# Kernel optimization log

Hardware: AMD Instinct MI355X
Metric: run time of the kernel (lower is better)

The kernel has to match this reference:

```python
import jax, jax.numpy as jnp
import numpy as np

EPS = 1e-07


def _softsplat(tenIn, tenFlow):
    # tenIn: [N, C, H, W], tenFlow: [N, 2, H, W]
    N, C, H, W = tenIn.shape
    dtype = tenIn.dtype
    gridX = jnp.arange(W, dtype=dtype)[None, None, :]  # [1,1,W]
    gridY = jnp.arange(H, dtype=dtype)[None, :, None]  # [1,H,1]
    fltX = gridX + tenFlow[:, 0]  # [N,H,W]
    fltY = gridY + tenFlow[:, 1]  # [N,H,W]
    finite = jnp.isfinite(fltX) & jnp.isfinite(fltY)
    fltX = jnp.where(finite, fltX, 0.0)
    fltY = jnp.where(finite, fltY, 0.0)
    nwX = jnp.floor(fltX)
    nwY = jnp.floor(fltY)
    b = jnp.arange(N, dtype=jnp.int32)[:, None, None]  # [N,1,1]
    tenIn_flat = jnp.transpose(tenIn, (0, 2, 3, 1)).reshape(-1, C)  # [N*H*W, C]
    out = jnp.zeros((N * H * W, C), dtype=dtype)
    # four bilinear corners: NW, NE, SW, SE
    for dx, dy in ((0, 0), (1, 0), (0, 1), (1, 1)):
        ix = nwX + dx
        iy = nwY + dy
        # bilinear weight, e.g. NW: (nwX+1-fltX)*(nwY+1-fltY)
        w = (1.0 - jnp.abs(fltX - ix)) * (1.0 - jnp.abs(fltY - iy))
        valid = finite & (ix >= 0) & (ix < W) & (iy >= 0) & (iy < H)
        w = jnp.where(valid, w, 0.0)  # zero-weight replaces torch's masked select
        ixi = jnp.clip(ix.astype(jnp.int32), 0, W - 1)
        iyi = jnp.clip(iy.astype(jnp.int32), 0, H - 1)
        idx = (b * (H * W) + iyi * W + ixi).reshape(-1)  # [N*H*W]
        out = out.at[idx].add(tenIn_flat * w.reshape(-1, 1))
    return jnp.transpose(out.reshape(N, H, W, C), (0, 3, 1, 2))


def setup_inputs() -> dict:
    key = jax.random.key(0)
    k1, k2, k3 = jax.random.split(key, 3)
    N, C, H, W = 4, 3, 1080, 1920
    tenIn = jax.random.normal(k1, (N, C, H, W), dtype=jnp.float32)
    tenFlow = jax.random.normal(k2, (N, 2, H, W), dtype=jnp.float32)
    tenMetric = jax.random.normal(k3, (N, 1, H, W), dtype=jnp.float32)
    return {"tenIn": tenIn, "tenFlow": tenFlow, "tenMetric": tenMetric}


def reference(tenIn, tenFlow, tenMetric):
    # mode='soft': concat [tenIn * exp(metric), exp(metric)], splat, normalize
    m = jnp.exp(tenMetric)
    tenCat = jnp.concatenate([tenIn * m, m], axis=1)  # [N, C+1, H, W]
    tenOut = _softsplat(tenCat, tenFlow)
    # mode_sub is None -> addeps normalization
    return tenOut[:, :-1] / (tenOut[:, -1:] + EPS)
```

## Files before the change

### kernel.cpp

```cpp
#include <hip/hip_runtime.h>
#include <math.h>

#define EPS 1e-7f

constexpr int Nn = 4, Hh = 1080, Ww = 1920;
constexpr int HW = Hh * Ww;
constexpr int TOTAL = Nn * HW;

constexpr int TW = 32, TH = 32;
constexpr int TXN = 60, TYN = 34;
constexpr int REACH = 5;
constexpr float NEAR_MAX = 5.0f;
constexpr int WINW = TW + 2 * REACH;
constexpr int WINH = TH + 2 * REACH;
constexpr int WINSZ = WINW * WINH;
constexpr int NCH = TH + 1;
constexpr int NCWc = TW + 1;
constexpr int NCELLS = NCWc * NCH;
constexpr int NOFF = NCELLS + 1;
constexpr int PADL = 8;
constexpr int NCHUNK = 12;
constexpr int TOTCH = NCHUNK * WINH;
constexpr float INV64K = 1.52587890625e-5f;


__global__ __launch_bounds__(256) void far_scatter(
    const float* __restrict__ tenIn, const float* __restrict__ tenFlow,
    const float* __restrict__ tenMetric,
    unsigned int* __restrict__ farCount, float* __restrict__ farList,
    unsigned int farCap)
{
    int q = blockIdx.x * 256 + threadIdx.x;
    if (q >= TOTAL / 4) return;
    int n  = q / (HW / 4);
    int p  = (q - n * (HW / 4)) * 4;

    const float* __restrict__ f0 = tenFlow + (size_t)(n * 2 + 0) * HW;
    const float* __restrict__ f1 = f0 + HW;
    float4 fx4 = *(const float4*)(f0 + p);
    float4 fy4 = *(const float4*)(f1 + p);

    float mx = fmaxf(fmaxf(fabsf(fx4.x), fabsf(fx4.y)), fmaxf(fabsf(fx4.z), fabsf(fx4.w)));
    float my = fmaxf(fmaxf(fabsf(fy4.x), fabsf(fy4.y)), fmaxf(fabsf(fy4.z), fabsf(fy4.w)));
    if (!(mx > NEAR_MAX || my > NEAR_MAX)) return;

    int y = p / Ww;
    int xbase = p - y * Ww;
    float fxa[4] = {fx4.x, fx4.y, fx4.z, fx4.w};
    float fya[4] = {fy4.x, fy4.y, fy4.z, fy4.w};

#pragma unroll
    for (int k = 0; k < 4; ++k) {
        float fxv = fxa[k], fyv = fya[k];
        if (!(fabsf(fxv) > NEAR_MAX || fabsf(fyv) > NEAR_MAX)) continue;
        float fx = (float)(xbase + k) + fxv;
        float fy = (float)y + fyv;
        if (!isfinite(fx) || !isfinite(fy)) continue;
        if (!(fx > -1.0f && fx < (float)Ww && fy > -1.0f && fy < (float)Hh)) continue;

        int pp = p + k;
        float m  = expf(tenMetric[(size_t)n * HW + pp]);
        float v0 = tenIn[((size_t)n * 3 + 0) * HW + pp] * m;
        float v1 = tenIn[((size_t)n * 3 + 1) * HW + pp] * m;
        float v2 = tenIn[((size_t)n * 3 + 2) * HW + pp] * m;

        unsigned int slot = atomicAdd(farCount, 1u);
        if (slot < farCap) {
            float* ep = farList + (size_t)slot * 8;
            ep[0] = __int_as_float(n);
            ep[1] = fx; ep[2] = fy;
            ep[3] = v0; ep[4] = v1; ep[5] = v2; ep[6] = m;
            ep[7] = 0.0f;
        }
    }
}


__global__ __launch_bounds__(256, 4) void gather_splat(
    const float* __restrict__ tenIn, const float* __restrict__ tenFlow,
    const float* __restrict__ tenMetric,
    const float* __restrict__ farList, const unsigned int* __restrict__ farCount,
    unsigned int farCap, float* __restrict__ out)
{
    __shared__ float4 sVal[WINSZ];
    __shared__ unsigned int sPack[WINSZ];
    __shared__ unsigned int sOff[NOFF];
    __shared__ unsigned int sWsum[8];

    const int tx = blockIdx.x, ty = blockIdx.y, n = blockIdx.z;
    const int tX = tx * TW, tY = ty * TH;
    const int tid = threadIdx.x;

    for (int j = tid; j < NOFF; j += 256) sOff[j] = 0u;
    __syncthreads();

    const float* __restrict__ f0 = tenFlow   + (size_t)(n * 2 + 0) * HW;
    const float* __restrict__ f1 = tenFlow   + (size_t)(n * 2 + 1) * HW;
    const float* __restrict__ mp = tenMetric + (size_t)n * HW;
    const float* __restrict__ i0 = tenIn + (size_t)(n * 3 + 0) * HW;
    const float* __restrict__ i1 = tenIn + (size_t)(n * 3 + 1) * HW;
    const float* __restrict__ i2 = tenIn + (size_t)(n * 3 + 2) * HW;

    unsigned int pk[2][4];
    unsigned int spw[2][4];
    float rv0[2][4], rv1[2][4], rv2[2][4], rvm[2][4];

#pragma unroll
    for (int cc = 0; cc < 2; ++cc) {
#pragma unroll
        for (int k = 0; k < 4; ++k) pk[cc][k] = 0xFFFFFFFFu;
        int cidx = tid + cc * 256;
        if (cidx >= TOTCH) continue;
        int wy = cidx / NCHUNK;
        int cx = cidx - wy * NCHUNK;
        int sy = tY - REACH + wy;
        int gx = tX - PADL + cx * 4;
        if (sy < 0 || sy >= Hh || gx < 0 || gx > Ww - 4) continue;
        int p = sy * Ww + gx;
        float4 fx4 = *(const float4*)(f0 + p);
        float4 fy4 = *(const float4*)(f1 + p);
        float4 m4  = *(const float4*)(mp + p);
        float4 a04 = *(const float4*)(i0 + p);
        float4 a14 = *(const float4*)(i1 + p);
        float4 a24 = *(const float4*)(i2 + p);
        float fxa[4] = {fx4.x, fx4.y, fx4.z, fx4.w};
        float fya[4] = {fy4.x, fy4.y, fy4.z, fy4.w};
        float ma[4]  = {m4.x,  m4.y,  m4.z,  m4.w};
        float a0a[4] = {a04.x, a04.y, a04.z, a04.w};
        float a1a[4] = {a14.x, a14.y, a14.z, a14.w};
        float a2a[4] = {a24.x, a24.y, a24.z, a24.w};
#pragma unroll
        for (int k = 0; k < 4; ++k) {
            int x = gx + k;
            if (x < tX - REACH || x >= tX + TW + REACH) continue;
            float fxv = fxa[k], fyv = fya[k];
            if (!(fabsf(fxv) <= NEAR_MAX && fabsf(fyv) <= NEAR_MAX)) continue;
            float fx = (float)x + fxv;
            float fy = (float)sy + fyv;
            float flx = floorf(fx), fly = floorf(fy);
            int lx0 = (int)flx - tX;
            int ly0 = (int)fly - tY;
            if (lx0 < -1 || lx0 >= TW || ly0 < -1 || ly0 >= TH) continue;
            int ci = (lx0 + 1) * NCH + (ly0 + 1);
            unsigned int sic = atomicAdd(&sOff[ci], 1u);
            pk[cc][k] = (sic << 16) | (unsigned int)ci;
            spw[cc][k] = __float2uint_rz((fx - flx) * 65536.0f)
                       | (__float2uint_rz((fy - fly) * 65536.0f) << 16);
            float m = expf(ma[k]);
            rv0[cc][k] = a0a[k] * m;
            rv1[cc][k] = a1a[k] * m;
            rv2[cc][k] = a2a[k] * m;
            rvm[cc][k] = m;
        }
    }
    __syncthreads();

    unsigned int c0v = 0, c1v = 0, c2v = 0, c3v = 0, c4v = 0;
    if (tid < 218) {
        int base = tid * 5;
        c0v = sOff[base];     c1v = sOff[base + 1]; c2v = sOff[base + 2];
        c3v = sOff[base + 3]; c4v = sOff[base + 4];
    }
    unsigned int tsum = c0v + c1v + c2v + c3v + c4v;
    unsigned int incl = tsum;
#pragma unroll
    for (int d = 1; d < 64; d <<= 1) {
        unsigned int v = __shfl_up(incl, d);
        if ((tid & 63) >= d) incl += v;
    }
    const int wv = tid >> 6;
    if ((tid & 63) == 63) sWsum[wv] = incl;
    __syncthreads();
    unsigned int woff = 0;
    {
        unsigned int w0 = sWsum[0], w1 = sWsum[1], w2 = sWsum[2];
        if (wv > 0) woff += w0;
        if (wv > 1) woff += w1;
        if (wv > 2) woff += w2;
    }
    unsigned int texcl = woff + incl - tsum;
    if (tid < 218) {
        int base = tid * 5;
        unsigned int o0 = texcl, o1 = o0 + c0v, o2 = o1 + c1v, o3 = o2 + c2v, o4 = o3 + c3v;
        sOff[base] = o0; sOff[base + 1] = o1; sOff[base + 2] = o2;
        sOff[base + 3] = o3; sOff[base + 4] = o4;
    }
    __syncthreads();

#pragma unroll
    for (int cc = 0; cc < 2; ++cc) {
#pragma unroll
        for (int k = 0; k < 4; ++k) {
            unsigned int p_ = pk[cc][k];
            if (p_ == 0xFFFFFFFFu) continue;
            unsigned int ci  = p_ & 0xFFFFu;
            unsigned int sic = p_ >> 16;
            unsigned int slot = sOff[ci] + sic;
            sPack[slot] = spw[cc][k];
            sVal[slot]  = make_float4(rv0[cc][k], rv1[cc][k], rv2[cc][k], rvm[cc][k]);
        }
    }
    __syncthreads();

    const int r   = tid >> 3;
    const int g   = tid & 7;
    const int cc0 = g * 4;

    float4 acc0 = make_float4(0.f, 0.f, 0.f, 0.f);
    float4 acc1 = make_float4(0.f, 0.f, 0.f, 0.f);
    float4 acc2 = make_float4(0.f, 0.f, 0.f, 0.f);
    float4 acc3 = make_float4(0.f, 0.f, 0.f, 0.f);

#define COLRANGE(J, HASL, HASR, ACCL, ACCR)                               \
    {                                                                     \
        const int cbase = (cc0 + (J)) * NCH + r;                          \
        unsigned int lo = sOff[cbase], md = sOff[cbase + 1],              \
                     hi = sOff[cbase + 2];                                \
        for (unsigned int s = lo; s < hi; ++s) {                          \
            unsigned int pw = sPack[s];                                   \
            float4 v = sVal[s];                                           \
            float fracx = (float)(pw & 0xFFFFu) * INV64K;                 \
            float wy1q  = (float)(pw >> 16)     * INV64K;                 \
            float ay = (s < md) ? wy1q : (1.0f - wy1q);                   \
            float wr = ay * fracx;                                        \
            float wl = ay - wr;                                           \
            if (HASL) { ACCL.x += v.x*wl; ACCL.y += v.y*wl;               \
                        ACCL.z += v.z*wl; ACCL.w += v.w*wl; }             \
            if (HASR) { ACCR.x += v.x*wr; ACCR.y += v.y*wr;               \
                        ACCR.z += v.z*wr; ACCR.w += v.w*wr; }             \
        }                                                                 \
    }

    COLRANGE(0, false, true,  acc0, acc0)
    COLRANGE(1, true,  true,  acc0, acc1)
    COLRANGE(2, true,  true,  acc1, acc2)
    COLRANGE(3, true,  true,  acc2, acc3)
    COLRANGE(4, true,  false, acc3, acc0)
#undef COLRANGE

    const int gy = tY + r;
    if (gy >= Hh) return;
    const int gx = tX + cc0;

    unsigned int fc = *farCount;
    if (fc > farCap) fc = farCap;
    const float gyf = (float)gy;
    const float gxf = (float)gx;
    for (unsigned int e = 0; e < fc; ++e) {
        const float* ep = farList + (size_t)e * 8;
        if (__float_as_int(ep[0]) != n) continue;
        float ffx = ep[1], ffy = ep[2];
        float ay = fmaxf(0.f, 1.f - fabsf(ffy - gyf));
        if (ay > 0.f) {
            float fv0 = ep[3], fv1 = ep[4], fv2 = ep[5], fm = ep[6];
            float d = ffx - gxf;
            float ax0 = fmaxf(0.f, 1.f - fabsf(d));
            float ax1 = fmaxf(0.f, 1.f - fabsf(d - 1.f));
            float ax2 = fmaxf(0.f, 1.f - fabsf(d - 2.f));
            float ax3 = fmaxf(0.f, 1.f - fabsf(d - 3.f));
            float w0 = ay * ax0, w1 = ay * ax1, w2 = ay * ax2, w3 = ay * ax3;
            acc0.x += fv0 * w0; acc0.y += fv1 * w0; acc0.z += fv2 * w0; acc0.w += fm * w0;
            acc1.x += fv0 * w1; acc1.y += fv1 * w1; acc1.z += fv2 * w1; acc1.w += fm * w1;
            acc2.x += fv0 * w2; acc2.y += fv1 * w2; acc2.z += fv2 * w2; acc2.w += fm * w2;
            acc3.x += fv0 * w3; acc3.y += fv1 * w3; acc3.z += fv2 * w3; acc3.w += fm * w3;
        }
    }

    const float inv0 = 1.0f / (acc0.w + EPS);
    const float inv1 = 1.0f / (acc1.w + EPS);
    const float inv2 = 1.0f / (acc2.w + EPS);
    const float inv3 = 1.0f / (acc3.w + EPS);

    const size_t pix = (size_t)gy * Ww + gx;
    float4 o;
    o = make_float4(acc0.x * inv0, acc1.x * inv1, acc2.x * inv2, acc3.x * inv3);
    *(float4*)(out + ((size_t)n * 3 + 0) * HW + pix) = o;
    o = make_float4(acc0.y * inv0, acc1.y * inv1, acc2.y * inv2, acc3.y * inv3);
    *(float4*)(out + ((size_t)n * 3 + 1) * HW + pix) = o;
    o = make_float4(acc0.z * inv0, acc1.z * inv1, acc2.z * inv2, acc3.z * inv3);
    *(float4*)(out + ((size_t)n * 3 + 2) * HW + pix) = o;
}

extern "C" void kernel_launch(void* const* d_in, const int* in_sizes, int n_in,
                              void* d_out, int out_size, void* d_ws, size_t ws_size,
                              hipStream_t stream) {
    const float* tenIn     = (const float*)d_in[0];
    const float* tenFlow   = (const float*)d_in[1];
    const float* tenMetric = (const float*)d_in[2];
    float* out = (float*)d_out;

    unsigned int* farCount = (unsigned int*)d_ws;
    float* farList = (float*)((char*)d_ws + 64);
    unsigned int farCap = (ws_size > 64) ? (unsigned int)((ws_size - 64) / 32) : 0;

    hipMemsetAsync(d_ws, 0, 64, stream);

    far_scatter<<<(TOTAL / 4 + 255) / 256, 256, 0, stream>>>(
        tenIn, tenFlow, tenMetric, farCount, farList, farCap);

    dim3 grid(TXN, TYN, Nn);
    gather_splat<<<grid, 256, 0, stream>>>(
        tenIn, tenFlow, tenMetric, farList, farCount, farCap, out);
}
```

Measured before the change: 299.3 us.

## Remap tiles per XCD and defer metric/input loads to valid chunks

Switches the gather kernel to a 1D grid, remapped so that consecutive tiles land on the same XCD, which should improve L2 reuse of the overlapping halo windows. The metric and three input-channel loads now happen only when at least one of the four pixels in a chunk lands in the tile. The exp and the multiplies move past the prefix-scan barrier. This cuts wasted global reads, but float4 values stay live across the barrier, which may raise register pressure.

```diff
diff --git a/kernel.cpp b/kernel.cpp
--- a/kernel.cpp
+++ b/kernel.cpp
@@ -21,6 +21,9 @@
 constexpr int PADL = 8;
 constexpr int NCHUNK = 12;
 constexpr int TOTCH = NCHUNK * WINH;
+constexpr int NTILES = TXN * TYN * Nn;
+constexpr int NXCD = 8;
+constexpr int TPX = NTILES / NXCD;
 constexpr float INV64K = 1.52587890625e-5f;
 
 
@@ -87,7 +90,13 @@
     __shared__ unsigned int sOff[NOFF];
     __shared__ unsigned int sWsum[8];
 
-    const int tx = blockIdx.x, ty = blockIdx.y, n = blockIdx.z;
+    const int bid = blockIdx.x;
+    const int lin = (bid & (NXCD - 1)) * TPX + (bid >> 3);
+    const int tx  = lin % TXN;
+    const int rem = lin / TXN;
+    const int ty  = rem % TYN;
+    const int n   = rem / TYN;
+
     const int tX = tx * TW, tY = ty * TH;
     const int tid = threadIdx.x;
 
@@ -103,7 +112,7 @@
 
     unsigned int pk[2][4];
     unsigned int spw[2][4];
-    float rv0[2][4], rv1[2][4], rv2[2][4], rvm[2][4];
+    float4 rm4[2], ra0[2], ra1[2], ra2[2];
 
 #pragma unroll
     for (int cc = 0; cc < 2; ++cc) {
@@ -119,16 +128,8 @@
         int p = sy * Ww + gx;
         float4 fx4 = *(const float4*)(f0 + p);
         float4 fy4 = *(const float4*)(f1 + p);
-        float4 m4  = *(const float4*)(mp + p);
-        float4 a04 = *(const float4*)(i0 + p);
-        float4 a14 = *(const float4*)(i1 + p);
-        float4 a24 = *(const float4*)(i2 + p);
         float fxa[4] = {fx4.x, fx4.y, fx4.z, fx4.w};
         float fya[4] = {fy4.x, fy4.y, fy4.z, fy4.w};
-        float ma[4]  = {m4.x,  m4.y,  m4.z,  m4.w};
-        float a0a[4] = {a04.x, a04.y, a04.z, a04.w};
-        float a1a[4] = {a14.x, a14.y, a14.z, a14.w};
-        float a2a[4] = {a24.x, a24.y, a24.z, a24.w};
 #pragma unroll
         for (int k = 0; k < 4; ++k) {
             int x = gx + k;
@@ -146,11 +147,13 @@
             pk[cc][k] = (sic << 16) | (unsigned int)ci;
             spw[cc][k] = __float2uint_rz((fx - flx) * 65536.0f)
                        | (__float2uint_rz((fy - fly) * 65536.0f) << 16);
-            float m = expf(ma[k]);
-            rv0[cc][k] = a0a[k] * m;
-            rv1[cc][k] = a1a[k] * m;
-            rv2[cc][k] = a2a[k] * m;
-            rvm[cc][k] = m;
+        }
+        unsigned int allv = pk[cc][0] & pk[cc][1] & pk[cc][2] & pk[cc][3];
+        if (allv != 0xFFFFFFFFu) {
+            rm4[cc] = *(const float4*)(mp + p);
+            ra0[cc] = *(const float4*)(i0 + p);
+            ra1[cc] = *(const float4*)(i1 + p);
+            ra2[cc] = *(const float4*)(i2 + p);
         }
     }
     __syncthreads();
@@ -189,6 +192,12 @@
 
 #pragma unroll
     for (int cc = 0; cc < 2; ++cc) {
+        unsigned int allv = pk[cc][0] & pk[cc][1] & pk[cc][2] & pk[cc][3];
+        if (allv == 0xFFFFFFFFu) continue;
+        float ma[4]  = {rm4[cc].x, rm4[cc].y, rm4[cc].z, rm4[cc].w};
+        float a0a[4] = {ra0[cc].x, ra0[cc].y, ra0[cc].z, ra0[cc].w};
+        float a1a[4] = {ra1[cc].x, ra1[cc].y, ra1[cc].z, ra1[cc].w};
+        float a2a[4] = {ra2[cc].x, ra2[cc].y, ra2[cc].z, ra2[cc].w};
 #pragma unroll
         for (int k = 0; k < 4; ++k) {
             unsigned int p_ = pk[cc][k];
@@ -196,8 +205,9 @@
             unsigned int ci  = p_ & 0xFFFFu;
             unsigned int sic = p_ >> 16;
             unsigned int slot = sOff[ci] + sic;
+            float m = expf(ma[k]);
             sPack[slot] = spw[cc][k];
-            sVal[slot]  = make_float4(rv0[cc][k], rv1[cc][k], rv2[cc][k], rvm[cc][k]);
+            sVal[slot]  = make_float4(a0a[k] * m, a1a[k] * m, a2a[k] * m, m);
         }
     }
     __syncthreads();
@@ -298,7 +308,6 @@
     far_scatter<<<(TOTAL / 4 + 255) / 256, 256, 0, stream>>>(
         tenIn, tenFlow, tenMetric, farCount, farList, farCap);
 
-    dim3 grid(TXN, TYN, Nn);
-    gather_splat<<<grid, 256, 0, stream>>>(
+    gather_splat<<<NTILES, 256, 0, stream>>>(
         tenIn, tenFlow, tenMetric, farList, farCount, farCap, out);
 }
```

New measurement: 273.7 us. -8.5%, faster.
